# Optimization experiments

Measured on AMD Instinct MI355X. Metric: run time of the kernel, lower is better.

The kernel has to match this reference:

```python
import jax, jax.numpy as jnp
import numpy as np
import math

T = 120      # frame_num == audio_len == max_seq_len
D = 64       # hidden_layer_size
H = 2        # n_head
DH = D // H
DFF = 2 * D
DOUT = 31
PERIOD = 10
EPS = 1e-5
NEG = -1e9
SCALE = 1.0 / math.sqrt(DH)
SLOPES = (1.0 / 16.0, 1.0 / 256.0)  # ALiBi slopes for n_head=2


def _pe():
    # PeriodicPositionalEncoding: sinusoid over one period, tiled
    pos = jnp.arange(PERIOD, dtype=jnp.float32)[:, None]
    div = jnp.exp(jnp.arange(0, D, 2, dtype=jnp.float32) * (-math.log(10000.0) / D))
    s, c = jnp.sin(pos * div), jnp.cos(pos * div)
    pe = jnp.stack([s, c], axis=-1).reshape(PERIOD, D)  # interleave sin/cos
    return jnp.tile(pe, (T // PERIOD + 1, 1))[:T]


def _alibi_mask():
    # causal mask + ALiBi bias: alibi[i,j] = -slope * floor((i-j)/period) for j<=i
    slopes = jnp.array(SLOPES, dtype=jnp.float32)
    i = jnp.arange(T)[:, None]
    j = jnp.arange(T)[None, :]
    rel = ((i - j) // PERIOD).astype(jnp.float32)
    return jnp.where(j <= i, -slopes[:, None, None] * rel, NEG)  # [H,T,T]


def _ln(x, g, b):
    m = x.mean(-1, keepdims=True)
    v = ((x - m) ** 2).mean(-1, keepdims=True)
    return (x - m) / jnp.sqrt(v + EPS) * g + b


def setup_inputs() -> dict:
    key = jax.random.key(0)
    ks = iter(jax.random.split(key, 32))
    n = lambda shape, s=0.05: jax.random.normal(next(ks), shape, dtype=jnp.float32) * s
    inp = {
        'audio': jax.random.normal(next(ks), (1, T, 1024), dtype=jnp.float32),
        'W_audio': n((D, 1024)), 'b_audio': n((D,)),
        'obj_W': n((D, 5)),
        'Wq': n((D, D)), 'bq': n((D,)), 'Wk': n((D, D)), 'bk': n((D,)),
        'Wv': n((D, D)), 'bv': n((D,)), 'Wo': n((D, D)), 'bo': n((D,)),
        'Wv2': n((D, D)), 'bv2': n((D,)), 'Wo2': n((D, D)), 'bo2': n((D,)),
        'g1': jnp.ones((D,)), 'be1': jnp.zeros((D,)),
        'g2': jnp.ones((D,)), 'be2': jnp.zeros((D,)),
        'g3': jnp.ones((D,)), 'be3': jnp.zeros((D,)),
        'W1': n((DFF, D)), 'c1': n((DFF,)), 'W2': n((D, DFF)), 'c2': n((D,)),
        'Wr': n((DOUT, D)), 'br': n((DOUT,)), 'Wm': n((D, DOUT)), 'bm': n((D,)),
    }
    return inp


def _forward(audio, W_audio, b_audio, obj_W, Wq, bq, Wk, bk, Wv, bv, Wo, bo,
             Wv2, bv2, Wo2, bo2, g1, be1, g2, be2, g3, be3,
             W1, c1, W2, c2, Wr, br, Wm, bm):
    mem = audio[0] @ W_audio.T + b_audio          # [S,D], S == T
    style = obj_W[:, 0]                            # obj_vector @ [1,0,0,0,0]
    pe = _pe()
    mask = _alibi_mask()
    slopes = jnp.array(SLOPES, dtype=jnp.float32)
    jarr = jnp.arange(T)

    # enc_dec_mask leaves exactly one memory key per target row (anti-diagonal
    # from the end); the feedback row t at step t always attends memory[-1],
    # so its cross-attn output is just the projected value of the last frame.
    cross_last = (mem[-1] @ Wv2.T + bv2) @ Wo2.T + bo2  # [D]

    def step(emb, t):
        # decode only the last row (row t) of the growing sequence; 1-layer
        # post-norm decoder => row t depends only on input rows 0..t.
        x = emb + pe                                 # PPE over prefix
        xq = jnp.take(x, t, axis=0)                  # [D]
        q = (xq @ Wq.T + bq).reshape(H, DH)
        k = (x @ Wk.T + bk).reshape(T, H, DH)
        v = (x @ Wv.T + bv).reshape(T, H, DH)
        bias = jnp.where(jarr <= t,
                         -slopes[:, None] * ((t - jarr) // PERIOD).astype(jnp.float32),
                         NEG)                        # [H,T]
        sc = jnp.einsum('hd,shd->hs', q, k) * SCALE + bias
        a = jax.nn.softmax(sc, axis=-1)
        sa = jnp.einsum('hs,shd->hd', a, v).reshape(D) @ Wo.T + bo
        h1 = _ln(xq + sa, g1, be1)
        h2 = _ln(h1 + cross_last, g2, be2)
        h3 = _ln(h2 + jax.nn.relu(h2 @ W1.T + c1) @ W2.T + c2, g3, be3)
        new = (h3 @ Wr.T + br) @ Wm.T + bm + style   # vertice_map(vertice_map_r(.)) + style
        emb = jax.lax.dynamic_update_slice(emb, new[None, :], (t + 1, 0))
        return emb, None

    emb0 = jnp.zeros((T, D), audio.dtype).at[0].set(style)
    emb, _ = jax.lax.scan(step, emb0, jnp.arange(T - 1))

    # final full-length decode (last loop iteration of the torch module)
    x = emb + pe
    q = (x @ Wq.T + bq).reshape(T, H, DH)
    k = (x @ Wk.T + bk).reshape(T, H, DH)
    v = (x @ Wv.T + bv).reshape(T, H, DH)
    sc = jnp.einsum('thd,shd->hts', q, k) * SCALE + mask
    a = jax.nn.softmax(sc, axis=-1)
    sa = jnp.einsum('hts,shd->thd', a, v).reshape(T, D) @ Wo.T + bo
    h1 = _ln(x + sa, g1, be1)
    # at length T with S == T the enc_dec_mask aligns target row j <-> memory row j
    cross = (mem @ Wv2.T + bv2) @ Wo2.T + bo2
    h2 = _ln(h1 + cross, g2, be2)
    h3 = _ln(h2 + jax.nn.relu(h2 @ W1.T + c1) @ W2.T + c2, g3, be3)
    return (h3 @ Wr.T + br)[None]                    # [1,T,31]


def reference(audio, W_audio, b_audio, obj_W, Wq, bq, Wk, bk, Wv, bv, Wo, bo,
              Wv2, bv2, Wo2, bo2, g1, be1, g2, be2, g3, be3,
              W1, c1, W2, c2, Wr, br, Wm, bm):
    return _forward(audio, W_audio, b_audio, obj_W, Wq, bq, Wk, bk, Wv, bv, Wo, bo,
                    Wv2, bv2, Wo2, bo2, g1, be1, g2, be2, g3, be3,
                    W1, c1, W2, c2, Wr, br, Wm, bm)
```

## Files before the change

### kernel.cpp

```cpp
#include <hip/hip_runtime.h>

typedef unsigned short u16;
typedef unsigned int   u32;
typedef _Float16 f16;
typedef f16 h2 __attribute__((ext_vector_type(2)));
typedef f16 h4 __attribute__((ext_vector_type(4)));
typedef f16 h8 __attribute__((ext_vector_type(8)));

#define T_    120
#define D_    64
#define DOUT_ 31
#define KROW_ 68
#define VROW_ 132

#if defined(__has_builtin)
#if __has_builtin(__builtin_amdgcn_fdot2)
#define DOT2(a,b,c) __builtin_amdgcn_fdot2((a),(b),(c),false)
#endif
#endif
#ifndef DOT2
#define DOT2(a,b,c) ((float)(a).x*(float)(b).x + ((float)(a).y*(float)(b).y + (c)))
#endif
#define SHV(x,i,j) __builtin_shufflevector((x),(x),(i),(j))

__device__ __forceinline__ h2 pk(float a, float b){
#if defined(__has_builtin) && __has_builtin(__builtin_amdgcn_cvt_pkrtz)
  return __builtin_bit_cast(h2, __builtin_amdgcn_cvt_pkrtz(a, b));
#else
  h2 r; r.x = (f16)a; r.y = (f16)b; return r;
#endif
}
__device__ __forceinline__ float b2f(u16 u){ return __uint_as_float(((u32)u) << 16); }
__device__ __forceinline__ float2 bp2(u32 u){
  float2 r; r.x = __uint_as_float(u << 16); r.y = __uint_as_float(u & 0xffff0000u); return r;
}
__device__ __forceinline__ u16 f2bu(float f){
  u32 u = __float_as_uint(f);
  u32 r = u + 0x7fffu + ((u >> 16) & 1u);
  return (u16)(r >> 16);
}
__device__ __forceinline__ u16 f2h16(float x){
  f16 v = (f16)x; u16 r; __builtin_memcpy(&r, &v, 2); return r;
}
#define WSYNC() do{ __asm__ __volatile__("" ::: "memory"); __builtin_amdgcn_wave_barrier(); }while(0)

__device__ __forceinline__ float dpp_sum(float x){
  int t;
  t = __builtin_amdgcn_update_dpp(0, __float_as_int(x), 0x111, 0xf, 0xf, true); x += __int_as_float(t);
  t = __builtin_amdgcn_update_dpp(0, __float_as_int(x), 0x112, 0xf, 0xf, true); x += __int_as_float(t);
  t = __builtin_amdgcn_update_dpp(0, __float_as_int(x), 0x114, 0xf, 0xf, true); x += __int_as_float(t);
  t = __builtin_amdgcn_update_dpp(0, __float_as_int(x), 0x118, 0xf, 0xf, true); x += __int_as_float(t);
  t = __builtin_amdgcn_update_dpp(0, __float_as_int(x), 0x142, 0xf, 0xf, true); x += __int_as_float(t);
  t = __builtin_amdgcn_update_dpp(0, __float_as_int(x), 0x143, 0xf, 0xf, true); x += __int_as_float(t);
  return __int_as_float(__builtin_amdgcn_readlane(__float_as_int(x), 63));
}
__device__ __forceinline__ float dpp_max_pos(float x){
  int t;
  t = __builtin_amdgcn_update_dpp(0, __float_as_int(x), 0x111, 0xf, 0xf, true); x = fmaxf(x, __int_as_float(t));
  t = __builtin_amdgcn_update_dpp(0, __float_as_int(x), 0x112, 0xf, 0xf, true); x = fmaxf(x, __int_as_float(t));
  t = __builtin_amdgcn_update_dpp(0, __float_as_int(x), 0x114, 0xf, 0xf, true); x = fmaxf(x, __int_as_float(t));
  t = __builtin_amdgcn_update_dpp(0, __float_as_int(x), 0x118, 0xf, 0xf, true); x = fmaxf(x, __int_as_float(t));
  t = __builtin_amdgcn_update_dpp(0, __float_as_int(x), 0x142, 0xf, 0xf, true); x = fmaxf(x, __int_as_float(t));
  t = __builtin_amdgcn_update_dpp(0, __float_as_int(x), 0x143, 0xf, 0xf, true); x = fmaxf(x, __int_as_float(t));
  return __int_as_float(__builtin_amdgcn_readlane(__float_as_int(x), 63));
}
__device__ __forceinline__ float pe_val(int row, int i){
  const float coef = -0.28782313662425574f;
  int p = row % 10;
  float dv  = __expf((float)(i >> 1) * coef);
  float ang = (float)p * dv;
  return (i & 1) ? __cosf(ang) : __sinf(ang);
}
__device__ __forceinline__ void loadrow32(h2* dst, const float* row){
  #pragma unroll
  for (int r = 0; r < 16; ++r){
    float4 f = ((const float4*)row)[r];
    dst[2*r]   = pk(f.x, f.y);
    dst[2*r+1] = pk(f.z, f.w);
  }
}

__global__ __launch_bounds__(256) void k_pre(const float* __restrict__ audio,
                                             const float* __restrict__ Wa, const float* __restrict__ ba,
                                             const float* __restrict__ Wv2, const float* __restrict__ bv2,
                                             const float* __restrict__ Wo2, const float* __restrict__ bo2,
                                             const float* __restrict__ Wo, const float* __restrict__ W1,
                                             const float* __restrict__ W2, const float* __restrict__ Wr,
                                             const float* __restrict__ Wm, const float* __restrict__ br,
                                             const float* __restrict__ bm,
                                             float* __restrict__ cross, float* __restrict__ Ms,
                                             float* __restrict__ bMv,
                                             u16* __restrict__ wob, u16* __restrict__ w1b,
                                             u16* __restrict__ w2b, u16* __restrict__ wrb){
  const int b = blockIdx.x, tid = threadIdx.x;
  if (b == 120){
    for (int i = tid; i < 4096; i += 256) wob[i] = f2bu(Wo[i]);
    for (int i = tid; i < 8192; i += 256){ w1b[i] = f2bu(W1[i]); w2b[i] = f2bu(W2[i]); }
    for (int i = tid; i < 1984; i += 256) wrb[i] = f2bu(Wr[i]);
    for (int idx = tid; idx < 4096; idx += 256){
      int d = idx >> 6, e = idx & 63;
      float acc = 0.f;
      #pragma unroll
      for (int j = 0; j < 31; ++j) acc += Wm[d*31 + j] * Wr[j*64 + e];
      Ms[idx] = acc;
    }
    if (tid < 64){
      float acc = bm[tid];
      #pragma unroll
      for (int j = 0; j < 31; ++j) acc += Wm[tid*31 + j] * br[j];
      bMv[tid] = acc;
    }
    return;
  }
  __shared__ float ash[1024];
  __shared__ float msh[64], tsh[64];
  for (int i = tid; i < 1024; i += 256) ash[i] = audio[b*1024 + i];
  __syncthreads();
  const int w = tid >> 6, lane = tid & 63;
  for (int d = w*16; d < w*16 + 16; ++d){
    const float4* row = (const float4*)(Wa + d*1024);
    float acc = 0.f;
    #pragma unroll
    for (int m = 0; m < 4; ++m){
      float4 wp = row[lane + 64*m];
      int j = 4*(lane + 64*m);
      acc += wp.x*ash[j] + wp.y*ash[j+1] + wp.z*ash[j+2] + wp.w*ash[j+3];
    }
    acc = dpp_sum(acc);
    if (lane == 0) msh[d] = acc + ba[d];
  }
  __syncthreads();
  if (tid < 64){
    const float4* r1 = (const float4*)(Wv2 + tid*64);
    float a = bv2[tid];
    #pragma unroll
    for (int j = 0; j < 16; ++j){ float4 p = r1[j]; a += p.x*msh[4*j] + p.y*msh[4*j+1] + p.z*msh[4*j+2] + p.w*msh[4*j+3]; }
    tsh[tid] = a;
  }
  __syncthreads();
  if (tid < 64){
    const float4* r2 = (const float4*)(Wo2 + tid*64);
    float c = bo2[tid];
    #pragma unroll
    for (int j = 0; j < 16; ++j){ float4 p = r2[j]; c += p.x*tsh[4*j] + p.y*tsh[4*j+1] + p.z*tsh[4*j+2] + p.w*tsh[4*j+3]; }
    cross[b*64 + tid] = c;
  }
}

__global__ __launch_bounds__(128, 1) void k_scan(
    const float* __restrict__ objW,
    const float* __restrict__ Wq, const float* __restrict__ bq,
    const float* __restrict__ Wk, const float* __restrict__ bk,
    const float* __restrict__ Wv, const float* __restrict__ bv,
    const float* __restrict__ Wo, const float* __restrict__ bo,
    const float* __restrict__ g1, const float* __restrict__ be1,
    const float* __restrict__ g2, const float* __restrict__ be2,
    const float* __restrict__ g3, const float* __restrict__ be3,
    const float* __restrict__ W1, const float* __restrict__ c1,
    const float* __restrict__ W2, const float* __restrict__ c2,
    const float* __restrict__ Ms, const float* __restrict__ bMv,
    const float* __restrict__ cross,
    u16* __restrict__ xw16, u16* __restrict__ Kw16, u16* __restrict__ Vw16)
{
  __shared__ __align__(16) f16 KcS[128*KROW_];
  __shared__ __align__(16) f16 VcS[D_*VROW_];
  __shared__ __align__(16) f16 xwS[T_*D_];
  __shared__ __align__(16) f16 sch[256];
  __shared__ __align__(16) f16 xh[64], qh[64], ath[64], h2h[64], h3h[64];
  __shared__ __align__(16) f16 fsh[128];
  __shared__ float at_p1[64], h2f[64], xf[64];
  __shared__ float pe_tab[640];

  const int tid = threadIdx.x;
  const int i = tid & 63;
  const bool w0 = tid < 64;

  h2 A[32], B[32], C[32], D[32], E[32];
  float biasA=0.f, biasB=0.f, bo_r=0.f, c1r=0.f, c2_r=0.f, bmst=0.f, cls_r=0.f;
  float g1r=0.f,b1r=0.f,g2r=0.f,b2r=0.f,g3r=0.f,b3r=0.f;

  if (w0){
    loadrow32(A, Wq + i*64);
    loadrow32(B, Wv + i*64);
    loadrow32(C, Wo + i*64);
    loadrow32(D, W1 + i*64);
    biasA = bq[i]; biasB = bv[i]; bo_r = bo[i]; c1r = c1[i];
    g1r = g1[i]; b1r = be1[i]; g2r = g2[i]; b2r = be2[i];
    cls_r = cross[119*64 + i];
  } else {
    loadrow32(A, Wk + i*64);
    loadrow32(B, W1 + (64+i)*64);
    loadrow32(C, W2 + i*128);
    loadrow32(D, W2 + i*128 + 64);
    loadrow32(E, Ms + i*64);
    biasA = bk[i]; c1r = c1[64+i]; c2_r = c2[i];
    g3r = g3[i]; b3r = be3[i];
    bmst = bMv[i] + objW[i*5];
  }
  { u32* p = (u32*)KcS; for (int idx = tid; idx < 128*KROW_/2; idx += 128) p[idx] = 0; }
  { u32* p = (u32*)VcS; for (int idx = tid; idx < D_*VROW_/2;  idx += 128) p[idx] = 0; }
  for (int idx = tid; idx < 640; idx += 128) pe_tab[idx] = pe_val(idx >> 6, idx & 63);
  if (w0){
    float st = objW[i*5];
    float x0 = st + pe_val(0, i);
    xf[i] = x0; xh[i] = (f16)x0; xwS[i] = (f16)x0;
  }
  __syncthreads();

  int pp = 1;
  for (int t = 0; t < T_-1; ++t){
    {
      const h8* xv = (const h8*)xh;
      if (w0){
        float q0=biasA,q1=0.f,q2=0.f,q3=0.f, v0=biasB,v1=0.f,v2=0.f,v3=0.f;
        #pragma unroll
        for (int r = 0; r < 8; ++r){
          h8 x = xv[r];
          h2 xa=SHV(x,0,1), xb=SHV(x,2,3), xc=SHV(x,4,5), xd=SHV(x,6,7);
          q0 = DOT2(A[4*r+0], xa, q0); q1 = DOT2(A[4*r+1], xb, q1);
          q2 = DOT2(A[4*r+2], xc, q2); q3 = DOT2(A[4*r+3], xd, q3);
          v0 = DOT2(B[4*r+0], xa, v0); v1 = DOT2(B[4*r+1], xb, v1);
          v2 = DOT2(B[4*r+2], xc, v2); v3 = DOT2(B[4*r+3], xd, v3);
        }
        qh[i] = (f16)((q0+q1)+(q2+q3));
        VcS[i*VROW_ + t] = (f16)((v0+v1)+(v2+v3));
      } else {
        float k0=biasA,k1=0.f,k2=0.f,k3=0.f;
        #pragma unroll
        for (int r = 0; r < 8; ++r){
          h8 x = xv[r];
          k0 = DOT2(A[4*r+0], SHV(x,0,1), k0);
          k1 = DOT2(A[4*r+1], SHV(x,2,3), k1);
          k2 = DOT2(A[4*r+2], SHV(x,4,5), k2);
          k3 = DOT2(A[4*r+3], SHV(x,6,7), k3);
        }
        KcS[t*KROW_ + i] = (f16)((k0+k1)+(k2+k3));
      }
    }
    __syncthreads();
    {
      const int h = tid >> 6, j = i;
      const h8* qv = (const h8*)(qh + h*32);
      const h4* k0 = (const h4*)(KcS + j*KROW_ + h*32);
      const h4* k1 = (const h4*)(KcS + (j+64)*KROW_ + h*32);
      float d0a=0.f,d0b=0.f,d1a=0.f,d1b=0.f;
      #pragma unroll
      for (int r = 0; r < 4; ++r){
        h8 q = qv[r];
        h4 ka = k0[2*r], kb = k0[2*r+1], kc = k1[2*r], kd = k1[2*r+1];
        d0a = DOT2(SHV(ka,0,1), SHV(q,0,1), d0a);
        d0b = DOT2(SHV(ka,2,3), SHV(q,2,3), d0b);
        d0a = DOT2(SHV(kb,0,1), SHV(q,4,5), d0a);
        d0b = DOT2(SHV(kb,2,3), SHV(q,6,7), d0b);
        d1a = DOT2(SHV(kc,0,1), SHV(q,0,1), d1a);
        d1b = DOT2(SHV(kc,2,3), SHV(q,2,3), d1b);
        d1a = DOT2(SHV(kd,0,1), SHV(q,4,5), d1a);
        d1b = DOT2(SHV(kd,2,3), SHV(q,6,7), d1b);
      }
      float d0 = d0a + d0b, d1 = d1a + d1b;
      const float slope = h ? 0.00390625f : 0.0625f;
      int r0 = (t - j) / 10, r1 = (t - j - 64) / 10;
      float s0 = (j      <= t) ? d0*0.17677669529663687f - slope*(float)r0 : -1e30f;
      float s1 = (j + 64 <= t) ? d1*0.17677669529663687f - slope*(float)r1 : -1e30f;
      float m = dpp_max_pos(fmaxf(s0, s1) + 16384.f) - 16384.f;
      float e0 = (j      <= t) ? __expf(s0 - m) : 0.f;
      float e1 = (j + 64 <= t) ? __expf(s1 - m) : 0.f;
      float inv = 1.f / dpp_sum(e0 + e1);
      sch[h*128 + j]      = (f16)(e0*inv);
      sch[h*128 + j + 64] = (f16)(e1*inv);
    }
    __syncthreads();
    float atp0 = 0.f;
    {
      const int hd = i >> 5;
      const h8* av = (const h8*)(sch + hd*128) + (w0 ? 0 : 8);
      const h4* vv = (const h4*)(VcS + i*VROW_) + (w0 ? 0 : 16);
      float p0=0.f,p1=0.f,p2=0.f,p3=0.f;
      #pragma unroll
      for (int r = 0; r < 8; ++r){
        h8 a = av[r];
        h4 va = vv[2*r], vb = vv[2*r+1];
        p0 = DOT2(SHV(va,0,1), SHV(a,0,1), p0);
        p1 = DOT2(SHV(va,2,3), SHV(a,2,3), p1);
        p2 = DOT2(SHV(vb,0,1), SHV(a,4,5), p2);
        p3 = DOT2(SHV(vb,2,3), SHV(a,6,7), p3);
      }
      float p = (p0+p1)+(p2+p3);
      if (!w0) at_p1[i] = p; else atp0 = p;
    }
    __syncthreads();
    if (w0){
      float atv = atp0 + at_p1[i];
      ath[i] = (f16)atv;
      WSYNC();
      const h8* av = (const h8*)ath;
      float a0=bo_r, a1=0.f, a2=0.f, a3=0.f;
      #pragma unroll
      for (int r = 0; r < 8; ++r){
        h8 x = av[r];
        a0 = DOT2(C[4*r+0], SHV(x,0,1), a0);
        a1 = DOT2(C[4*r+1], SHV(x,2,3), a1);
        a2 = DOT2(C[4*r+2], SHV(x,4,5), a2);
        a3 = DOT2(C[4*r+3], SHV(x,6,7), a3);
      }
      float y = xf[i] + (a0+a1)+(a2+a3);
      float s = dpp_sum(y), s2 = dpp_sum(y*y);
      float m = s*(1.f/64.f), var = fmaxf(s2*(1.f/64.f) - m*m, 0.f);
      float h1 = (y - m)*rsqrtf(var + 1e-5f)*g1r + b1r;
      float z = h1 + cls_r;
      float sz = dpp_sum(z), sz2 = dpp_sum(z*z);
      float mz = sz*(1.f/64.f), vz = fmaxf(sz2*(1.f/64.f) - mz*mz, 0.f);
      float h2v = (z - mz)*rsqrtf(vz + 1e-5f)*g2r + b2r;
      h2h[i] = (f16)h2v;
      h2f[i] = h2v;
    }
    __syncthreads();
    {
      const h8* hv = (const h8*)h2h;
      float a0=c1r, a1=0.f, a2=0.f, a3=0.f;
      if (w0){
        #pragma unroll
        for (int r = 0; r < 8; ++r){
          h8 x = hv[r];
          a0 = DOT2(D[4*r+0], SHV(x,0,1), a0);
          a1 = DOT2(D[4*r+1], SHV(x,2,3), a1);
          a2 = DOT2(D[4*r+2], SHV(x,4,5), a2);
          a3 = DOT2(D[4*r+3], SHV(x,6,7), a3);
        }
      } else {
        #pragma unroll
        for (int r = 0; r < 8; ++r){
          h8 x = hv[r];
          a0 = DOT2(B[4*r+0], SHV(x,0,1), a0);
          a1 = DOT2(B[4*r+1], SHV(x,2,3), a1);
          a2 = DOT2(B[4*r+2], SHV(x,4,5), a2);
          a3 = DOT2(B[4*r+3], SHV(x,6,7), a3);
        }
      }
      fsh[tid] = (f16)fmaxf((a0+a1)+(a2+a3), 0.f);
    }
    __syncthreads();
    if (!w0){
      const h8* fv = (const h8*)fsh;
      float a0=c2_r, a1=0.f, a2=0.f, a3=0.f;
      #pragma unroll
      for (int r = 0; r < 8; ++r){
        h8 x = fv[r];
        a0 = DOT2(C[4*r+0], SHV(x,0,1), a0);
        a1 = DOT2(C[4*r+1], SHV(x,2,3), a1);
        a2 = DOT2(C[4*r+2], SHV(x,4,5), a2);
        a3 = DOT2(C[4*r+3], SHV(x,6,7), a3);
      }
      #pragma unroll
      for (int r = 0; r < 8; ++r){
        h8 x = fv[8+r];
        a0 = DOT2(D[4*r+0], SHV(x,0,1), a0);
        a1 = DOT2(D[4*r+1], SHV(x,2,3), a1);
        a2 = DOT2(D[4*r+2], SHV(x,4,5), a2);
        a3 = DOT2(D[4*r+3], SHV(x,6,7), a3);
      }
      float y = h2f[i] + (a0+a1)+(a2+a3);
      float s = dpp_sum(y), s2 = dpp_sum(y*y);
      float m = s*(1.f/64.f), var = fmaxf(s2*(1.f/64.f) - m*m, 0.f);
      float h3v = (y - m)*rsqrtf(var + 1e-5f)*g3r + b3r;
      h3h[i] = (f16)h3v;
      WSYNC();
      const h8* hv3 = (const h8*)h3h;
      float m0=bmst, m1=0.f, m2=0.f, m3=0.f;
      #pragma unroll
      for (int r = 0; r < 8; ++r){
        h8 x = hv3[r];
        m0 = DOT2(E[4*r+0], SHV(x,0,1), m0);
        m1 = DOT2(E[4*r+1], SHV(x,2,3), m1);
        m2 = DOT2(E[4*r+2], SHV(x,4,5), m2);
        m3 = DOT2(E[4*r+3], SHV(x,6,7), m3);
      }
      float xn = (m0+m1)+(m2+m3) + pe_tab[pp*64 + i];
      xf[i] = xn;
      xh[i] = (f16)xn;
      xwS[(t+1)*64 + i] = (f16)xn;
    }
    __syncthreads();
    pp = (pp == 9) ? 0 : pp + 1;
  }
  {
    const h8* xv = (const h8*)xh;
    if (w0){
      float v0=biasB,v1=0.f,v2=0.f,v3=0.f;
      #pragma unroll
      for (int r = 0; r < 8; ++r){
        h8 x = xv[r];
        v0 = DOT2(B[4*r+0], SHV(x,0,1), v0);
        v1 = DOT2(B[4*r+1], SHV(x,2,3), v1);
        v2 = DOT2(B[4*r+2], SHV(x,4,5), v2);
        v3 = DOT2(B[4*r+3], SHV(x,6,7), v3);
      }
      Vw16[119*64 + i] = f2h16((v0+v1)+(v2+v3));
    } else {
      float k0=biasA,k1=0.f,k2=0.f,k3=0.f;
      #pragma unroll
      for (int r = 0; r < 8; ++r){
        h8 x = xv[r];
        k0 = DOT2(A[4*r+0], SHV(x,0,1), k0);
        k1 = DOT2(A[4*r+1], SHV(x,2,3), k1);
        k2 = DOT2(A[4*r+2], SHV(x,4,5), k2);
        k3 = DOT2(A[4*r+3], SHV(x,6,7), k3);
      }
      Kw16[119*64 + i] = f2h16((k0+k1)+(k2+k3));
    }
  }
  {
    const u16* kc = (const u16*)KcS;
    const u16* vc = (const u16*)VcS;
    for (int idx = tid; idx < 119*64; idx += 128){
      int t_ = idx >> 6, d = idx & 63;
      Kw16[idx] = kc[t_*KROW_ + d];
      Vw16[idx] = vc[d*VROW_ + t_];
    }
    const u32* xs32 = (const u32*)xwS;
    for (int idx = tid; idx < T_*D_/2; idx += 128) ((u32*)xw16)[idx] = xs32[idx];
  }
}

__global__ __launch_bounds__(128) void k_final(
    const float* __restrict__ Wq, const float* __restrict__ bq, const float* __restrict__ bo,
    const float* __restrict__ g1, const float* __restrict__ be1,
    const float* __restrict__ g2, const float* __restrict__ be2,
    const float* __restrict__ g3, const float* __restrict__ be3,
    const float* __restrict__ c1, const float* __restrict__ c2, const float* __restrict__ br,
    const u16* __restrict__ wo_b, const u16* __restrict__ w1_b,
    const u16* __restrict__ w2_b, const u16* __restrict__ wr_b,
    const float* __restrict__ cross, const u16* __restrict__ xw16,
    const u16* __restrict__ Kw16, const u16* __restrict__ Vw16,
    float* __restrict__ out)
{
  __shared__ float xs[64], qs[64], at[64], h2s[64], h3s[64], fs[128], sc[256];
  const int irow = blockIdx.x, tid = threadIdx.x;
  const f16* xp = (const f16*)xw16;
  const f16* kp = (const f16*)Kw16;
  const f16* vp = (const f16*)Vw16;
  if (tid < 64) xs[tid] = (float)xp[irow*64 + tid];
  __syncthreads();
  if (tid < 64){
    const float4* wr_ = (const float4*)(Wq + tid*64);
    float acc = bq[tid];
    #pragma unroll
    for (int j = 0; j < 16; ++j){ float4 w = wr_[j]; acc += w.x*xs[4*j] + w.y*xs[4*j+1] + w.z*xs[4*j+2] + w.w*xs[4*j+3]; }
    qs[tid] = acc;
  }
  __syncthreads();
  {
    const int h = tid >> 6, j = tid & 63;
    const float* qh_ = qs + h*32;
    float d0 = 0.f, d1 = 0.f;
    const h4* k0 = (const h4*)(kp + j*64 + h*32);
    #pragma unroll
    for (int w = 0; w < 8; ++w){
      h4 p = k0[w];
      d0 += (float)p.x*qh_[4*w] + (float)p.y*qh_[4*w+1] + (float)p.z*qh_[4*w+2] + (float)p.w*qh_[4*w+3];
    }
    if (j < 56){
      const h4* k1 = (const h4*)(kp + (j+64)*64 + h*32);
      #pragma unroll
      for (int w = 0; w < 8; ++w){
        h4 p = k1[w];
        d1 += (float)p.x*qh_[4*w] + (float)p.y*qh_[4*w+1] + (float)p.z*qh_[4*w+2] + (float)p.w*qh_[4*w+3];
      }
    }
    const float slope = h ? 0.00390625f : 0.0625f;
    float s0 = (j      <= irow) ? d0*0.17677669529663687f - slope*(float)((irow-j)/10)    : -1e30f;
    float s1 = (j + 64 <= irow) ? d1*0.17677669529663687f - slope*(float)((irow-j-64)/10) : -1e30f;
    float m = dpp_max_pos(fmaxf(s0, s1) + 16384.f) - 16384.f;
    float e0 = (j      <= irow) ? __expf(s0 - m) : 0.f;
    float e1 = (j + 64 <= irow) ? __expf(s1 - m) : 0.f;
    float inv = 1.f / dpp_sum(e0 + e1);
    sc[h*128 + j]      = e0*inv;
    sc[h*128 + j + 64] = e1*inv;
  }
  __syncthreads();
  if (tid < 64){
    const float* a = sc + (tid >> 5)*128;
    float a0=0.f,a1=0.f,a2=0.f,a3=0.f;
    #pragma unroll
    for (int jj = 0; jj < 30; ++jj){
      a0 += a[4*jj]   * (float)vp[(4*jj)*64   + tid];
      a1 += a[4*jj+1] * (float)vp[(4*jj+1)*64 + tid];
      a2 += a[4*jj+2] * (float)vp[(4*jj+2)*64 + tid];
      a3 += a[4*jj+3] * (float)vp[(4*jj+3)*64 + tid];
    }
    at[tid] = (a0+a1)+(a2+a3);
  }
  __syncthreads();
  if (tid < 64){
    const u32* orow = (const u32*)(wo_b + tid*64);
    float acc = bo[tid];
    #pragma unroll
    for (int w = 0; w < 32; ++w){ float2 p = bp2(orow[w]); acc += p.x*at[2*w] + p.y*at[2*w+1]; }
    float y = xs[tid] + acc;
    float s = dpp_sum(y), s2 = dpp_sum(y*y);
    float m = s*(1.f/64.f), var = fmaxf(s2*(1.f/64.f) - m*m, 0.f);
    float h1 = (y - m)*rsqrtf(var + 1e-5f)*g1[tid] + be1[tid];
    float z = h1 + cross[irow*64 + tid];
    float sz = dpp_sum(z), sz2 = dpp_sum(z*z);
    float mz = sz*(1.f/64.f), vz = fmaxf(sz2*(1.f/64.f) - mz*mz, 0.f);
    h2s[tid] = (z - mz)*rsqrtf(vz + 1e-5f)*g2[tid] + be2[tid];
  }
  __syncthreads();
  {
    const u32* w1r = (const u32*)(w1_b + tid*64);
    float acc = c1[tid];
    #pragma unroll
    for (int w = 0; w < 32; ++w){ float2 p = bp2(w1r[w]); acc += p.x*h2s[2*w] + p.y*h2s[2*w+1]; }
    fs[tid] = fmaxf(acc, 0.f);
  }
  __syncthreads();
  if (tid < 64){
    const u32* w2r = (const u32*)(w2_b + tid*128);
    float acc = c2[tid];
    #pragma unroll
    for (int w = 0; w < 64; ++w){ float2 p = bp2(w2r[w]); acc += p.x*fs[2*w] + p.y*fs[2*w+1]; }
    float y = h2s[tid] + acc;
    float s = dpp_sum(y), s2 = dpp_sum(y*y);
    float m = s*(1.f/64.f), var = fmaxf(s2*(1.f/64.f) - m*m, 0.f);
    h3s[tid] = (y - m)*rsqrtf(var + 1e-5f)*g3[tid] + be3[tid];
  }
  __syncthreads();
  if (tid < DOUT_){
    const u32* rr = (const u32*)(wr_b + tid*64);
    float acc = br[tid];
    #pragma unroll
    for (int w = 0; w < 32; ++w){ float2 p = bp2(rr[w]); acc += p.x*h3s[2*w] + p.y*h3s[2*w+1]; }
    out[irow*DOUT_ + tid] = acc;
  }
}

extern "C" void kernel_launch(void* const* d_in, const int* in_sizes, int n_in,
                              void* d_out, int out_size, void* d_ws, size_t ws_size,
                              hipStream_t stream){
  const float* audio=(const float*)d_in[0];
  const float* Wa   =(const float*)d_in[1];
  const float* ba   =(const float*)d_in[2];
  const float* objW =(const float*)d_in[3];
  const float* Wq   =(const float*)d_in[4];
  const float* bq   =(const float*)d_in[5];
  const float* Wk   =(const float*)d_in[6];
  const float* bk   =(const float*)d_in[7];
  const float* Wv   =(const float*)d_in[8];
  const float* bv   =(const float*)d_in[9];
  const float* Wo   =(const float*)d_in[10];
  const float* bo   =(const float*)d_in[11];
  const float* Wv2  =(const float*)d_in[12];
  const float* bv2  =(const float*)d_in[13];
  const float* Wo2  =(const float*)d_in[14];
  const float* bo2  =(const float*)d_in[15];
  const float* g1   =(const float*)d_in[16];
  const float* be1  =(const float*)d_in[17];
  const float* g2   =(const float*)d_in[18];
  const float* be2  =(const float*)d_in[19];
  const float* g3   =(const float*)d_in[20];
  const float* be3  =(const float*)d_in[21];
  const float* W1   =(const float*)d_in[22];
  const float* c1   =(const float*)d_in[23];
  const float* W2   =(const float*)d_in[24];
  const float* c2   =(const float*)d_in[25];
  const float* Wr   =(const float*)d_in[26];
  const float* br   =(const float*)d_in[27];
  const float* Wm   =(const float*)d_in[28];
  const float* bm   =(const float*)d_in[29];

  float* ws    = (float*)d_ws;
  float* cross = ws;
  float* Ms    = ws + 7680;
  float* bMv   = ws + 11776;
  u16* xw16 = (u16*)(ws + 11840);
  u16* Kw16 = xw16 + 7680;
  u16* Vw16 = Kw16 + 7680;
  u16* wo_b = Vw16 + 7680;
  u16* w1_b = wo_b + 4096;
  u16* w2_b = w1_b + 8192;
  u16* wr_b = w2_b + 8192;
  float* out = (float*)d_out;

  k_pre  <<<dim3(121), dim3(256), 0, stream>>>(audio, Wa, ba, Wv2, bv2, Wo2, bo2,
                                               Wo, W1, W2, Wr, Wm, br, bm,
                                               cross, Ms, bMv, wo_b, w1_b, w2_b, wr_b);
  k_scan <<<dim3(1),   dim3(128), 0, stream>>>(objW, Wq, bq, Wk, bk, Wv, bv, Wo, bo,
                                               g1, be1, g2, be2, g3, be3,
                                               W1, c1, W2, c2, Ms, bMv,
                                               cross, xw16, Kw16, Vw16);
  k_final<<<dim3(120), dim3(128), 0, stream>>>(Wq, bq, bo, g1, be1, g2, be2, g3, be3,
                                               c1, c2, br, wo_b, w1_b, w2_b, wr_b,
                                               cross, xw16, Kw16, Vw16, out);
}
```

Baseline: 390.2 us.

## Split decode step into two-wave pipeline with one block barrier per step

Reorganizes the sequential decode loop so wave 0 runs V projection, both attention heads, softmax, the output projection with both layernorms, and the full FFN first layer. Wave 1 runs the FFN second layer, layernorm, memory projection, and the next step's Q/K projections. This cuts the block-wide barriers per step from six to two and uses cheaper intra-wave syncs for the rest. The softmax also drops the max-subtraction, which assumes the scores stay small enough not to overflow exp. W2 rows are repacked so the FFN output can be passed between waves as packed half pairs.

```diff
diff --git a/kernel.cpp b/kernel.cpp
--- a/kernel.cpp
+++ b/kernel.cpp
@@ -167,254 +167,272 @@
   __shared__ __align__(16) f16 xwS[T_*D_];
   __shared__ __align__(16) f16 sch[256];
   __shared__ __align__(16) f16 xh[64], qh[64], ath[64], h2h[64], h3h[64];
-  __shared__ __align__(16) f16 fsh[128];
-  __shared__ float at_p1[64], h2f[64], xf[64];
+  __shared__ __align__(16) h2  fsh2[64];
+  __shared__ float xf[64], h2f[64];
   __shared__ float pe_tab[640];
 
   const int tid = threadIdx.x;
   const int i = tid & 63;
   const bool w0 = tid < 64;
 
-  h2 A[32], B[32], C[32], D[32], E[32];
-  float biasA=0.f, biasB=0.f, bo_r=0.f, c1r=0.f, c2_r=0.f, bmst=0.f, cls_r=0.f;
+  h2 R0[32], R1[32], R2[32], R3[32], R4[32];
+  float bA=0.f, bB=0.f, c1a=0.f, c1b=0.f, c2r=0.f, bmst=0.f, cls_r=0.f;
   float g1r=0.f,b1r=0.f,g2r=0.f,b2r=0.f,g3r=0.f,b3r=0.f;
 
   if (w0){
-    loadrow32(A, Wq + i*64);
-    loadrow32(B, Wv + i*64);
-    loadrow32(C, Wo + i*64);
-    loadrow32(D, W1 + i*64);
-    biasA = bq[i]; biasB = bv[i]; bo_r = bo[i]; c1r = c1[i];
+    loadrow32(R0, Wv + i*64);
+    loadrow32(R1, Wo + i*64);
+    loadrow32(R2, W1 + i*64);
+    loadrow32(R3, W1 + (64+i)*64);
+    bA = bv[i]; bB = bo[i]; c1a = c1[i]; c1b = c1[64+i];
     g1r = g1[i]; b1r = be1[i]; g2r = g2[i]; b2r = be2[i];
     cls_r = cross[119*64 + i];
   } else {
-    loadrow32(A, Wk + i*64);
-    loadrow32(B, W1 + (64+i)*64);
-    loadrow32(C, W2 + i*128);
-    loadrow32(D, W2 + i*128 + 64);
-    loadrow32(E, Ms + i*64);
-    biasA = bk[i]; c1r = c1[64+i]; c2_r = c2[i];
+    loadrow32(R0, Wq + i*64);
+    loadrow32(R1, Wk + i*64);
+    {
+      const float4* ra = (const float4*)(W2 + i*128);
+      const float4* rb = (const float4*)(W2 + i*128 + 64);
+      #pragma unroll
+      for (int r = 0; r < 8; ++r){
+        float4 a = ra[r], b = rb[r];
+        R2[4*r+0] = pk(a.x, b.x); R2[4*r+1] = pk(a.y, b.y);
+        R2[4*r+2] = pk(a.z, b.z); R2[4*r+3] = pk(a.w, b.w);
+      }
+      #pragma unroll
+      for (int r = 0; r < 8; ++r){
+        float4 a = ra[8+r], b = rb[8+r];
+        R3[4*r+0] = pk(a.x, b.x); R3[4*r+1] = pk(a.y, b.y);
+        R3[4*r+2] = pk(a.z, b.z); R3[4*r+3] = pk(a.w, b.w);
+      }
+    }
+    loadrow32(R4, Ms + i*64);
+    bA = bq[i]; bB = bk[i]; c2r = c2[i];
     g3r = g3[i]; b3r = be3[i];
     bmst = bMv[i] + objW[i*5];
   }
   { u32* p = (u32*)KcS; for (int idx = tid; idx < 128*KROW_/2; idx += 128) p[idx] = 0; }
   { u32* p = (u32*)VcS; for (int idx = tid; idx < D_*VROW_/2;  idx += 128) p[idx] = 0; }
   for (int idx = tid; idx < 640; idx += 128) pe_tab[idx] = pe_val(idx >> 6, idx & 63);
-  if (w0){
+  __syncthreads();
+
+  if (!w0){
     float st = objW[i*5];
     float x0 = st + pe_val(0, i);
     xf[i] = x0; xh[i] = (f16)x0; xwS[i] = (f16)x0;
-  }
-  __syncthreads();
+    WSYNC();
+    const h8* xv = (const h8*)xh;
+    float q0=bA,q1=0.f,q2=0.f,q3=0.f, k0=bB,k1=0.f,k2=0.f,k3=0.f;
+    #pragma unroll
+    for (int r = 0; r < 8; ++r){
+      h8 x = xv[r];
+      h2 xa=SHV(x,0,1), xb=SHV(x,2,3), xc=SHV(x,4,5), xd=SHV(x,6,7);
+      q0 = DOT2(R0[4*r+0], xa, q0); q1 = DOT2(R0[4*r+1], xb, q1);
+      q2 = DOT2(R0[4*r+2], xc, q2); q3 = DOT2(R0[4*r+3], xd, q3);
+      k0 = DOT2(R1[4*r+0], xa, k0); k1 = DOT2(R1[4*r+1], xb, k1);
+      k2 = DOT2(R1[4*r+2], xc, k2); k3 = DOT2(R1[4*r+3], xd, k3);
+    }
+    qh[i] = (f16)((q0+q1)+(q2+q3));
+    KcS[i] = (f16)((k0+k1)+(k2+k3));
+  }
 
   int pp = 1;
   for (int t = 0; t < T_-1; ++t){
-    {
-      const h8* xv = (const h8*)xh;
-      if (w0){
-        float q0=biasA,q1=0.f,q2=0.f,q3=0.f, v0=biasB,v1=0.f,v2=0.f,v3=0.f;
+    __syncthreads();
+    if (w0){
+      {
+        const h8* xv = (const h8*)xh;
+        float v0=bA,v1=0.f,v2=0.f,v3=0.f;
+        #pragma unroll
+        for (int r = 0; r < 8; ++r){
+          h8 x = xv[r];
+          v0 = DOT2(R0[4*r+0], SHV(x,0,1), v0);
+          v1 = DOT2(R0[4*r+1], SHV(x,2,3), v1);
+          v2 = DOT2(R0[4*r+2], SHV(x,4,5), v2);
+          v3 = DOT2(R0[4*r+3], SHV(x,6,7), v3);
+        }
+        VcS[i*VROW_ + t] = (f16)((v0+v1)+(v2+v3));
+      }
+      WSYNC();
+      {
+        const h8* qv  = (const h8*)qh;
+        const h4* kr0 = (const h4*)(KcS + i*KROW_);
+        const h4* kr1 = (const h4*)(KcS + (i+64)*KROW_);
+        float d00a=0.f,d00b=0.f,d01a=0.f,d01b=0.f,d10a=0.f,d10b=0.f,d11a=0.f,d11b=0.f;
+        #pragma unroll
+        for (int r = 0; r < 4; ++r){
+          h8 ql = qv[r], qhn = qv[4+r];
+          h2 ql0=SHV(ql,0,1),  ql1=SHV(ql,2,3),  ql2=SHV(ql,4,5),  ql3=SHV(ql,6,7);
+          h2 qh0=SHV(qhn,0,1), qh1=SHV(qhn,2,3), qh2=SHV(qhn,4,5), qh3=SHV(qhn,6,7);
+          h4 ka = kr0[2*r],   kb = kr0[2*r+1];
+          h4 kc = kr0[8+2*r], kd = kr0[9+2*r];
+          h4 ke = kr1[2*r],   kf = kr1[2*r+1];
+          h4 kg = kr1[8+2*r], kh = kr1[9+2*r];
+          d00a = DOT2(SHV(ka,0,1), ql0, d00a); d00b = DOT2(SHV(ka,2,3), ql1, d00b);
+          d00a = DOT2(SHV(kb,0,1), ql2, d00a); d00b = DOT2(SHV(kb,2,3), ql3, d00b);
+          d10a = DOT2(SHV(kc,0,1), qh0, d10a); d10b = DOT2(SHV(kc,2,3), qh1, d10b);
+          d10a = DOT2(SHV(kd,0,1), qh2, d10a); d10b = DOT2(SHV(kd,2,3), qh3, d10b);
+          d01a = DOT2(SHV(ke,0,1), ql0, d01a); d01b = DOT2(SHV(ke,2,3), ql1, d01b);
+          d01a = DOT2(SHV(kf,0,1), ql2, d01a); d01b = DOT2(SHV(kf,2,3), ql3, d01b);
+          d11a = DOT2(SHV(kg,0,1), qh0, d11a); d11b = DOT2(SHV(kg,2,3), qh1, d11b);
+          d11a = DOT2(SHV(kh,0,1), qh2, d11a); d11b = DOT2(SHV(kh,2,3), qh3, d11b);
+        }
+        const float SC = 0.17677669529663687f;
+        int r0 = (t - i) / 10, r1 = (t - i - 64) / 10;
+        bool m0 = (i <= t), m1 = (i + 64 <= t);
+        float e00 = m0 ? __expf((d00a+d00b)*SC - 0.0625f*(float)r0)     : 0.f;
+        float e01 = m1 ? __expf((d01a+d01b)*SC - 0.0625f*(float)r1)     : 0.f;
+        float e10 = m0 ? __expf((d10a+d10b)*SC - 0.00390625f*(float)r0) : 0.f;
+        float e11 = m1 ? __expf((d11a+d11b)*SC - 0.00390625f*(float)r1) : 0.f;
+        float inv0 = 1.f / dpp_sum(e00 + e01);
+        float inv1 = 1.f / dpp_sum(e10 + e11);
+        sch[i]        = (f16)(e00*inv0);
+        sch[64+i]     = (f16)(e01*inv0);
+        sch[128+i]    = (f16)(e10*inv1);
+        sch[192+i]    = (f16)(e11*inv1);
+      }
+      WSYNC();
+      {
+        const h8* av = (const h8*)(sch + (i >> 5)*128);
+        const h4* vv = (const h4*)(VcS + i*VROW_);
+        float p0=0.f,p1=0.f,p2=0.f,p3=0.f;
+        #pragma unroll
+        for (int r = 0; r < 15; ++r){
+          h8 a = av[r];
+          h4 va = vv[2*r], vb = vv[2*r+1];
+          p0 = DOT2(SHV(va,0,1), SHV(a,0,1), p0);
+          p1 = DOT2(SHV(va,2,3), SHV(a,2,3), p1);
+          p2 = DOT2(SHV(vb,0,1), SHV(a,4,5), p2);
+          p3 = DOT2(SHV(vb,2,3), SHV(a,6,7), p3);
+        }
+        ath[i] = (f16)((p0+p1)+(p2+p3));
+      }
+      WSYNC();
+      {
+        const h8* av = (const h8*)ath;
+        float a0=bB, a1=0.f, a2=0.f, a3=0.f;
+        #pragma unroll
+        for (int r = 0; r < 8; ++r){
+          h8 x = av[r];
+          a0 = DOT2(R1[4*r+0], SHV(x,0,1), a0);
+          a1 = DOT2(R1[4*r+1], SHV(x,2,3), a1);
+          a2 = DOT2(R1[4*r+2], SHV(x,4,5), a2);
+          a3 = DOT2(R1[4*r+3], SHV(x,6,7), a3);
+        }
+        float y = xf[i] + (a0+a1)+(a2+a3);
+        float s = dpp_sum(y), s2 = dpp_sum(y*y);
+        float m = s*(1.f/64.f), var = fmaxf(s2*(1.f/64.f) - m*m, 0.f);
+        float h1 = (y - m)*rsqrtf(var + 1e-5f)*g1r + b1r;
+        float z = h1 + cls_r;
+        float sz = dpp_sum(z), sz2 = dpp_sum(z*z);
+        float mz = sz*(1.f/64.f), vz = fmaxf(sz2*(1.f/64.f) - mz*mz, 0.f);
+        float h2v = (z - mz)*rsqrtf(vz + 1e-5f)*g2r + b2r;
+        h2h[i] = (f16)h2v;
+        h2f[i] = h2v;
+      }
+      WSYNC();
+      {
+        const h8* hv = (const h8*)h2h;
+        float a0=c1a, a1=0.f, a2=0.f, a3=0.f, b0=c1b, b1=0.f, b2=0.f, b3=0.f;
+        #pragma unroll
+        for (int r = 0; r < 8; ++r){
+          h8 x = hv[r];
+          h2 xa=SHV(x,0,1), xb=SHV(x,2,3), xc=SHV(x,4,5), xd=SHV(x,6,7);
+          a0 = DOT2(R2[4*r+0], xa, a0); a1 = DOT2(R2[4*r+1], xb, a1);
+          a2 = DOT2(R2[4*r+2], xc, a2); a3 = DOT2(R2[4*r+3], xd, a3);
+          b0 = DOT2(R3[4*r+0], xa, b0); b1 = DOT2(R3[4*r+1], xb, b1);
+          b2 = DOT2(R3[4*r+2], xc, b2); b3 = DOT2(R3[4*r+3], xd, b3);
+        }
+        fsh2[i] = pk(fmaxf((a0+a1)+(a2+a3), 0.f), fmaxf((b0+b1)+(b2+b3), 0.f));
+      }
+    }
+    __syncthreads();
+    if (!w0){
+      float h3v;
+      {
+        const h8* fv = (const h8*)fsh2;
+        float a0=c2r, a1=0.f, a2=0.f, a3=0.f;
+        #pragma unroll
+        for (int r = 0; r < 8; ++r){
+          h8 x = fv[r];
+          a0 = DOT2(R2[4*r+0], SHV(x,0,1), a0);
+          a1 = DOT2(R2[4*r+1], SHV(x,2,3), a1);
+          a2 = DOT2(R2[4*r+2], SHV(x,4,5), a2);
+          a3 = DOT2(R2[4*r+3], SHV(x,6,7), a3);
+        }
+        #pragma unroll
+        for (int r = 0; r < 8; ++r){
+          h8 x = fv[8+r];
+          a0 = DOT2(R3[4*r+0], SHV(x,0,1), a0);
+          a1 = DOT2(R3[4*r+1], SHV(x,2,3), a1);
+          a2 = DOT2(R3[4*r+2], SHV(x,4,5), a2);
+          a3 = DOT2(R3[4*r+3], SHV(x,6,7), a3);
+        }
+        float y = h2f[i] + (a0+a1)+(a2+a3);
+        float s = dpp_sum(y), s2 = dpp_sum(y*y);
+        float m = s*(1.f/64.f), var = fmaxf(s2*(1.f/64.f) - m*m, 0.f);
+        h3v = (y - m)*rsqrtf(var + 1e-5f)*g3r + b3r;
+        h3h[i] = (f16)h3v;
+      }
+      WSYNC();
+      {
+        const h8* hv3 = (const h8*)h3h;
+        float m0=bmst, m1=0.f, m2=0.f, m3=0.f;
+        #pragma unroll
+        for (int r = 0; r < 8; ++r){
+          h8 x = hv3[r];
+          m0 = DOT2(R4[4*r+0], SHV(x,0,1), m0);
+          m1 = DOT2(R4[4*r+1], SHV(x,2,3), m1);
+          m2 = DOT2(R4[4*r+2], SHV(x,4,5), m2);
+          m3 = DOT2(R4[4*r+3], SHV(x,6,7), m3);
+        }
+        float xn = (m0+m1)+(m2+m3) + pe_tab[pp*64 + i];
+        xf[i] = xn;
+        xh[i] = (f16)xn;
+        xwS[(t+1)*64 + i] = (f16)xn;
+      }
+      WSYNC();
+      {
+        const h8* xv = (const h8*)xh;
+        float q0=bA,q1=0.f,q2=0.f,q3=0.f, k0=bB,k1=0.f,k2=0.f,k3=0.f;
         #pragma unroll
         for (int r = 0; r < 8; ++r){
           h8 x = xv[r];
           h2 xa=SHV(x,0,1), xb=SHV(x,2,3), xc=SHV(x,4,5), xd=SHV(x,6,7);
-          q0 = DOT2(A[4*r+0], xa, q0); q1 = DOT2(A[4*r+1], xb, q1);
-          q2 = DOT2(A[4*r+2], xc, q2); q3 = DOT2(A[4*r+3], xd, q3);
-          v0 = DOT2(B[4*r+0], xa, v0); v1 = DOT2(B[4*r+1], xb, v1);
-          v2 = DOT2(B[4*r+2], xc, v2); v3 = DOT2(B[4*r+3], xd, v3);
+          q0 = DOT2(R0[4*r+0], xa, q0); q1 = DOT2(R0[4*r+1], xb, q1);
+          q2 = DOT2(R0[4*r+2], xc, q2); q3 = DOT2(R0[4*r+3], xd, q3);
+          k0 = DOT2(R1[4*r+0], xa, k0); k1 = DOT2(R1[4*r+1], xb, k1);
+          k2 = DOT2(R1[4*r+2], xc, k2); k3 = DOT2(R1[4*r+3], xd, k3);
         }
         qh[i] = (f16)((q0+q1)+(q2+q3));
-        VcS[i*VROW_ + t] = (f16)((v0+v1)+(v2+v3));
-      } else {
-        float k0=biasA,k1=0.f,k2=0.f,k3=0.f;
-        #pragma unroll
-        for (int r = 0; r < 8; ++r){
-          h8 x = xv[r];
-          k0 = DOT2(A[4*r+0], SHV(x,0,1), k0);
-          k1 = DOT2(A[4*r+1], SHV(x,2,3), k1);
-          k2 = DOT2(A[4*r+2], SHV(x,4,5), k2);
-          k3 = DOT2(A[4*r+3], SHV(x,6,7), k3);
-        }
-        KcS[t*KROW_ + i] = (f16)((k0+k1)+(k2+k3));
-      }
-    }
-    __syncthreads();
-    {
-      const int h = tid >> 6, j = i;
-      const h8* qv = (const h8*)(qh + h*32);
-      const h4* k0 = (const h4*)(KcS + j*KROW_ + h*32);
-      const h4* k1 = (const h4*)(KcS + (j+64)*KROW_ + h*32);
-      float d0a=0.f,d0b=0.f,d1a=0.f,d1b=0.f;
-      #pragma unroll
-      for (int r = 0; r < 4; ++r){
-        h8 q = qv[r];
-        h4 ka = k0[2*r], kb = k0[2*r+1], kc = k1[2*r], kd = k1[2*r+1];
-        d0a = DOT2(SHV(ka,0,1), SHV(q,0,1), d0a);
-        d0b = DOT2(SHV(ka,2,3), SHV(q,2,3), d0b);
-        d0a = DOT2(SHV(kb,0,1), SHV(q,4,5), d0a);
-        d0b = DOT2(SHV(kb,2,3), SHV(q,6,7), d0b);
-        d1a = DOT2(SHV(kc,0,1), SHV(q,0,1), d1a);
-        d1b = DOT2(SHV(kc,2,3), SHV(q,2,3), d1b);
-        d1a = DOT2(SHV(kd,0,1), SHV(q,4,5), d1a);
-        d1b = DOT2(SHV(kd,2,3), SHV(q,6,7), d1b);
-      }
-      float d0 = d0a + d0b, d1 = d1a + d1b;
-      const float slope = h ? 0.00390625f : 0.0625f;
-      int r0 = (t - j) / 10, r1 = (t - j - 64) / 10;
-      float s0 = (j      <= t) ? d0*0.17677669529663687f - slope*(float)r0 : -1e30f;
-      float s1 = (j + 64 <= t) ? d1*0.17677669529663687f - slope*(float)r1 : -1e30f;
-      float m = dpp_max_pos(fmaxf(s0, s1) + 16384.f) - 16384.f;
-      float e0 = (j      <= t) ? __expf(s0 - m) : 0.f;
-      float e1 = (j + 64 <= t) ? __expf(s1 - m) : 0.f;
-      float inv = 1.f / dpp_sum(e0 + e1);
-      sch[h*128 + j]      = (f16)(e0*inv);
-      sch[h*128 + j + 64] = (f16)(e1*inv);
-    }
-    __syncthreads();
-    float atp0 = 0.f;
-    {
-      const int hd = i >> 5;
-      const h8* av = (const h8*)(sch + hd*128) + (w0 ? 0 : 8);
-      const h4* vv = (const h4*)(VcS + i*VROW_) + (w0 ? 0 : 16);
-      float p0=0.f,p1=0.f,p2=0.f,p3=0.f;
-      #pragma unroll
-      for (int r = 0; r < 8; ++r){
-        h8 a = av[r];
-        h4 va = vv[2*r], vb = vv[2*r+1];
-        p0 = DOT2(SHV(va,0,1), SHV(a,0,1), p0);
-        p1 = DOT2(SHV(va,2,3), SHV(a,2,3), p1);
-        p2 = DOT2(SHV(vb,0,1), SHV(a,4,5), p2);
-        p3 = DOT2(SHV(vb,2,3), SHV(a,6,7), p3);
-      }
-      float p = (p0+p1)+(p2+p3);
-      if (!w0) at_p1[i] = p; else atp0 = p;
-    }
-    __syncthreads();
-    if (w0){
-      float atv = atp0 + at_p1[i];
-      ath[i] = (f16)atv;
-      WSYNC();
-      const h8* av = (const h8*)ath;
-      float a0=bo_r, a1=0.f, a2=0.f, a3=0.f;
-      #pragma unroll
-      for (int r = 0; r < 8; ++r){
-        h8 x = av[r];
-        a0 = DOT2(C[4*r+0], SHV(x,0,1), a0);
-        a1 = DOT2(C[4*r+1], SHV(x,2,3), a1);
-        a2 = DOT2(C[4*r+2], SHV(x,4,5), a2);
-        a3 = DOT2(C[4*r+3], SHV(x,6,7), a3);
-      }
-      float y = xf[i] + (a0+a1)+(a2+a3);
-      float s = dpp_sum(y), s2 = dpp_sum(y*y);
-      float m = s*(1.f/64.f), var = fmaxf(s2*(1.f/64.f) - m*m, 0.f);
-      float h1 = (y - m)*rsqrtf(var + 1e-5f)*g1r + b1r;
-      float z = h1 + cls_r;
-      float sz = dpp_sum(z), sz2 = dpp_sum(z*z);
-      float mz = sz*(1.f/64.f), vz = fmaxf(sz2*(1.f/64.f) - mz*mz, 0.f);
-      float h2v = (z - mz)*rsqrtf(vz + 1e-5f)*g2r + b2r;
-      h2h[i] = (f16)h2v;
-      h2f[i] = h2v;
-    }
-    __syncthreads();
-    {
-      const h8* hv = (const h8*)h2h;
-      float a0=c1r, a1=0.f, a2=0.f, a3=0.f;
-      if (w0){
-        #pragma unroll
-        for (int r = 0; r < 8; ++r){
-          h8 x = hv[r];
-          a0 = DOT2(D[4*r+0], SHV(x,0,1), a0);
-          a1 = DOT2(D[4*r+1], SHV(x,2,3), a1);
-          a2 = DOT2(D[4*r+2], SHV(x,4,5), a2);
-          a3 = DOT2(D[4*r+3], SHV(x,6,7), a3);
-        }
-      } else {
-        #pragma unroll
-        for (int r = 0; r < 8; ++r){
-          h8 x = hv[r];
-          a0 = DOT2(B[4*r+0], SHV(x,0,1), a0);
-          a1 = DOT2(B[4*r+1], SHV(x,2,3), a1);
-          a2 = DOT2(B[4*r+2], SHV(x,4,5), a2);
-          a3 = DOT2(B[4*r+3], SHV(x,6,7), a3);
-        }
-      }
-      fsh[tid] = (f16)fmaxf((a0+a1)+(a2+a3), 0.f);
-    }
-    __syncthreads();
-    if (!w0){
-      const h8* fv = (const h8*)fsh;
-      float a0=c2_r, a1=0.f, a2=0.f, a3=0.f;
-      #pragma unroll
-      for (int r = 0; r < 8; ++r){
-        h8 x = fv[r];
-        a0 = DOT2(C[4*r+0], SHV(x,0,1), a0);
-        a1 = DOT2(C[4*r+1], SHV(x,2,3), a1);
-        a2 = DOT2(C[4*r+2], SHV(x,4,5), a2);
-        a3 = DOT2(C[4*r+3], SHV(x,6,7), a3);
-      }
-      #pragma unroll
-      for (int r = 0; r < 8; ++r){
-        h8 x = fv[8+r];
-        a0 = DOT2(D[4*r+0], SHV(x,0,1), a0);
-        a1 = DOT2(D[4*r+1], SHV(x,2,3), a1);
-        a2 = DOT2(D[4*r+2], SHV(x,4,5), a2);
-        a3 = DOT2(D[4*r+3], SHV(x,6,7), a3);
-      }
-      float y = h2f[i] + (a0+a1)+(a2+a3);
-      float s = dpp_sum(y), s2 = dpp_sum(y*y);
-      float m = s*(1.f/64.f), var = fmaxf(s2*(1.f/64.f) - m*m, 0.f);
-      float h3v = (y - m)*rsqrtf(var + 1e-5f)*g3r + b3r;
-      h3h[i] = (f16)h3v;
-      WSYNC();
-      const h8* hv3 = (const h8*)h3h;
-      float m0=bmst, m1=0.f, m2=0.f, m3=0.f;
-      #pragma unroll
-      for (int r = 0; r < 8; ++r){
-        h8 x = hv3[r];
-        m0 = DOT2(E[4*r+0], SHV(x,0,1), m0);
-        m1 = DOT2(E[4*r+1], SHV(x,2,3), m1);
-        m2 = DOT2(E[4*r+2], SHV(x,4,5), m2);
-        m3 = DOT2(E[4*r+3], SHV(x,6,7), m3);
-      }
-      float xn = (m0+m1)+(m2+m3) + pe_tab[pp*64 + i];
-      xf[i] = xn;
-      xh[i] = (f16)xn;
-      xwS[(t+1)*64 + i] = (f16)xn;
-    }
-    __syncthreads();
+        KcS[(t+1)*KROW_ + i] = (f16)((k0+k1)+(k2+k3));
+      }
+    }
     pp = (pp == 9) ? 0 : pp + 1;
   }
-  {
+  __syncthreads();
+  if (w0){
     const h8* xv = (const h8*)xh;
-    if (w0){
-      float v0=biasB,v1=0.f,v2=0.f,v3=0.f;
-      #pragma unroll
-      for (int r = 0; r < 8; ++r){
-        h8 x = xv[r];
-        v0 = DOT2(B[4*r+0], SHV(x,0,1), v0);
-        v1 = DOT2(B[4*r+1], SHV(x,2,3), v1);
-        v2 = DOT2(B[4*r+2], SHV(x,4,5), v2);
-        v3 = DOT2(B[4*r+3], SHV(x,6,7), v3);
-      }
-      Vw16[119*64 + i] = f2h16((v0+v1)+(v2+v3));
-    } else {
-      float k0=biasA,k1=0.f,k2=0.f,k3=0.f;
-      #pragma unroll
-      for (int r = 0; r < 8; ++r){
-        h8 x = xv[r];
-        k0 = DOT2(A[4*r+0], SHV(x,0,1), k0);
-        k1 = DOT2(A[4*r+1], SHV(x,2,3), k1);
-        k2 = DOT2(A[4*r+2], SHV(x,4,5), k2);
-        k3 = DOT2(A[4*r+3], SHV(x,6,7), k3);
-      }
-      Kw16[119*64 + i] = f2h16((k0+k1)+(k2+k3));
-    }
+    float v0=bA,v1=0.f,v2=0.f,v3=0.f;
+    #pragma unroll
+    for (int r = 0; r < 8; ++r){
+      h8 x = xv[r];
+      v0 = DOT2(R0[4*r+0], SHV(x,0,1), v0);
+      v1 = DOT2(R0[4*r+1], SHV(x,2,3), v1);
+      v2 = DOT2(R0[4*r+2], SHV(x,4,5), v2);
+      v3 = DOT2(R0[4*r+3], SHV(x,6,7), v3);
+    }
+    Vw16[119*64 + i] = f2h16((v0+v1)+(v2+v3));
   }
   {
     const u16* kc = (const u16*)KcS;
     const u16* vc = (const u16*)VcS;
+    for (int idx = tid; idx < 120*64; idx += 128){
+      int t_ = idx >> 6, d = idx & 63;
+      Kw16[idx] = kc[t_*KROW_ + d];
+    }
     for (int idx = tid; idx < 119*64; idx += 128){
       int t_ = idx >> 6, d = idx & 63;
-      Kw16[idx] = kc[t_*KROW_ + d];
       Vw16[idx] = vc[d*VROW_ + t_];
     }
     const u32* xs32 = (const u32*)xwS;
```

After: 411.4 us. 5.4% more time.
